# Performance work log

Measured on AMD Instinct MI355X. Metric: run time of the kernel, lower is better.

## Reference

```python
import jax, jax.numpy as jnp
import numpy as np

G, K, CG = 4, 9, 16        # DCNv3 groups, kernel points (3x3), channels/group
C = G * CG                 # internal channels = 64
OUT = 64                   # out_channels
B, H, W = 2, 256, 256


def _conv(x, w, b):  # NCHW / OIHW, SAME, stride 1
    y = jax.lax.conv_general_dilated(x, w, (1, 1), 'SAME',
                                     dimension_numbers=('NCHW', 'OIHW', 'NCHW'))
    return y + b[None, :, None, None]


def _fourdir2xy(sd):
    # rotate the two diagonal SD gradient channels by 45 deg into x/y gradients
    d0, d1 = sd[:, 0:1], sd[:, 1:2]
    return (d0 + d1) * 0.5, (d1 - d0) * 0.5


def _poisson(gx, gy, iters=20):
    # laplacian_blending_1c_batch: Jacobi Poisson solve from gradient field
    z = jnp.zeros_like(gx[:, :, :, :1])
    dgx = gx - jnp.concatenate([z, gx[:, :, :, :-1]], axis=3)
    zy = jnp.zeros_like(gy[:, :, :1, :])
    dgy = gy - jnp.concatenate([zy, gy[:, :, :-1, :]], axis=2)
    div = dgx + dgy

    def step(i, u):
        up = jnp.pad(u, ((0, 0), (0, 0), (1, 1), (1, 1)), mode='edge')
        nbr = (up[:, :, :-2, 1:-1] + up[:, :, 2:, 1:-1]
               + up[:, :, 1:-1, :-2] + up[:, :, 1:-1, 2:])
        return (nbr - div) * 0.25

    return jax.lax.fori_loop(0, iters, step, jnp.zeros_like(div))


def _dcnv3(cop, aop, W_in, b_in, W_aop, b_aop, dw, W_off, b_off,
           W_mask, b_mask, W_out, b_out):
    # channels-last DCNv3: COP provides features, AOP drives offsets/masks
    x = cop @ W_in + b_in                      # [B,H,W,C]
    a = jax.nn.gelu(aop @ W_aop + b_aop)       # [B,H,W,C]
    a = jax.lax.conv_general_dilated(a, dw, (1, 1), 'SAME',
                                     dimension_numbers=('NHWC', 'HWIO', 'NHWC'),
                                     feature_group_count=C)
    a = jax.nn.gelu(a)
    Bn, Hn, Wn = x.shape[0], x.shape[1], x.shape[2]
    off = (a @ W_off + b_off).reshape(Bn, Hn, Wn, G, K, 2)
    m = jax.nn.softmax((a @ W_mask + b_mask).reshape(Bn, Hn, Wn, G, K), axis=-1)
    xg = x.reshape(Bn, Hn, Wn, G, CG)
    yy, xx = jnp.meshgrid(jnp.arange(Hn, dtype=x.dtype),
                          jnp.arange(Wn, dtype=x.dtype), indexing='ij')
    k = jnp.arange(K)
    pky = (k // 3 - 1).astype(x.dtype)
    pkx = (k % 3 - 1).astype(x.dtype)
    ly = yy[None, :, :, None, None] + pky[None, None, None, None, :] + off[..., 0]
    lx = xx[None, :, :, None, None] + pkx[None, None, None, None, :] + off[..., 1]
    y0 = jnp.floor(ly)
    x0 = jnp.floor(lx)
    wy = ly - y0
    wx = lx - x0
    bi = jnp.arange(Bn)[:, None, None, None, None]
    gi = jnp.arange(G)[None, None, None, :, None]
    acc = jnp.zeros((Bn, Hn, Wn, G, CG), dtype=x.dtype)
    for dy, dx in ((0, 0), (0, 1), (1, 0), (1, 1)):
        yi = y0 + dy
        xi = x0 + dx
        wgt = (wy if dy else 1 - wy) * (wx if dx else 1 - wx)
        valid = ((yi >= 0) & (yi < Hn) & (xi >= 0) & (xi < Wn)).astype(x.dtype)
        yc = jnp.clip(yi, 0, Hn - 1).astype(jnp.int32)
        xc = jnp.clip(xi, 0, Wn - 1).astype(jnp.int32)
        v = xg[bi, yc, xc, gi]                  # [B,H,W,G,K,CG] gather
        acc = acc + jnp.einsum('bhwgk,bhwgkc->bhwgc', m * wgt * valid, v)
    return acc.reshape(Bn, Hn, Wn, C) @ W_out + b_out


def _forward(x, rw1, rb1, rw2, rb2, rw3, rb3, W_in, b_in, W_aop, b_aop, dw,
             W_off, b_off, W_mask, b_mask, W_out, b_out):
    img0 = x[:, 0:3]
    td = x[:, 3:5]
    sd1 = x[:, 5:7]
    sd0 = x[:, 7:9]
    Ix1, Iy1 = _fourdir2xy(sd1)
    gray = _poisson(-Ix1, -Iy1, 20)            # [B,1,H,W]
    h = jax.nn.silu(_conv(jnp.concatenate([img0, td, sd1], axis=1), rw1, rb1))
    h = jax.nn.silu(_conv(h, rw2, rb2))
    recon = _conv(h, rw3, rb3)                 # [B,3,H,W]
    core = jax.lax.stop_gradient(jnp.concatenate([img0, gray, recon], axis=1))
    guide = jax.lax.stop_gradient(jnp.concatenate([sd0, sd1], axis=1))
    cop = jnp.transpose(core, (0, 2, 3, 1))    # [B,H,W,7]
    aop = jnp.transpose(guide, (0, 2, 3, 1))   # [B,H,W,4]
    out = _dcnv3(cop, aop, W_in, b_in, W_aop, b_aop, dw, W_off, b_off,
                 W_mask, b_mask, W_out, b_out)
    return jnp.transpose(out, (0, 3, 1, 2))    # [B,OUT,H,W]


def setup_inputs() -> dict:
    key = jax.random.key(0)
    ks = jax.random.split(key, 20)
    d = {}
    d['x'] = jax.random.normal(ks[0], (B, 9, H, W), dtype=jnp.float32)
    # recon CNN (7 -> 32 -> 32 -> 3)
    d['rw1'] = jax.random.normal(ks[1], (32, 7, 3, 3), dtype=jnp.float32) * 0.1
    d['rb1'] = jnp.zeros((32,), jnp.float32)
    d['rw2'] = jax.random.normal(ks[2], (32, 32, 3, 3), dtype=jnp.float32) * 0.1
    d['rb2'] = jnp.zeros((32,), jnp.float32)
    d['rw3'] = jax.random.normal(ks[3], (3, 32, 3, 3), dtype=jnp.float32) * 0.1
    d['rb3'] = jnp.zeros((3,), jnp.float32)
    # DCNv3_Mod params
    d['W_in'] = jax.random.normal(ks[4], (7, C), dtype=jnp.float32) * 0.1
    d['b_in'] = jnp.zeros((C,), jnp.float32)
    d['W_aop'] = jax.random.normal(ks[5], (4, C), dtype=jnp.float32) * 0.1
    d['b_aop'] = jnp.zeros((C,), jnp.float32)
    d['dw'] = jax.random.normal(ks[6], (3, 3, 1, C), dtype=jnp.float32) * 0.1
    d['W_off'] = jax.random.normal(ks[7], (C, G * K * 2), dtype=jnp.float32) * 0.01
    d['b_off'] = jnp.zeros((G * K * 2,), jnp.float32)
    d['W_mask'] = jax.random.normal(ks[8], (C, G * K), dtype=jnp.float32) * 0.1
    d['b_mask'] = jnp.zeros((G * K,), jnp.float32)
    d['W_out'] = jax.random.normal(ks[9], (C, OUT), dtype=jnp.float32) * 0.1
    d['b_out'] = jnp.zeros((OUT,), jnp.float32)
    return d


def reference(x, rw1, rb1, rw2, rb2, rw3, rb3, W_in, b_in, W_aop, b_aop, dw,
              W_off, b_off, W_mask, b_mask, W_out, b_out):
    return _forward(x, rw1, rb1, rw2, rb2, rw3, rb3, W_in, b_in, W_aop, b_aop,
                    dw, W_off, b_off, W_mask, b_mask, W_out, b_out)
```

## Files before the change

### kernel.cpp

```cpp
#include <hip/hip_runtime.h>
#include <math.h>

#define H_ 256
#define W_ 256
#define HW_ 65536
#define BHW_ 131072
#define NPC 8388608

typedef __attribute__((ext_vector_type(8))) short short8v;
typedef __attribute__((ext_vector_type(4))) float f32x4;

__device__ __forceinline__ float geluf(float x) {
    const float k2 = 2.f * 0.7978845608028654f;
    float t2 = k2 * (x + 0.044715f * x * x * x);
    return x / (1.f + __expf(-t2));
}
__device__ __forceinline__ float siluf(float x) {
    return x / (1.f + __expf(-x));
}
__device__ __forceinline__ unsigned short f2bf(float f) {
    unsigned u = __float_as_uint(f);
    u = (u + 0x7FFF + ((u >> 16) & 1)) >> 16;
    return (unsigned short)u;
}

__device__ __forceinline__ float wcomb(const float* Woff, const float* Wmask, int c, int j) {
    return j < 72 ? Woff[c * 72 + j] : (j < 108 ? Wmask[c * 36 + (j - 72)] : 0.f);
}

__global__ __launch_bounds__(256) void k_mega(const float* __restrict__ x,
        float* __restrict__ gray,
        const float* __restrict__ Wa, const float* __restrict__ ba,
        const float* __restrict__ dwW, float* __restrict__ a2,
        const float* __restrict__ rw1, const float* __restrict__ rb1,
        float* __restrict__ h1,
        const float* __restrict__ Woff, const float* __restrict__ boff,
        const float* __restrict__ Wmask, const float* __restrict__ bmask,
        const float* __restrict__ Wout, const float* __restrict__ rw2,
        const float* __restrict__ rw3,
        unsigned short* __restrict__ WBpack, unsigned short* __restrict__ WOpack,
        unsigned short* __restrict__ WB2,
        float* __restrict__ bcomb, float* __restrict__ wT3) {
    __shared__ float smem[6400];
    int bid = blockIdx.x;
    int tid = threadIdx.x;

    if (bid < 512) {
        float* u = smem;
        float* dv = smem + 3192;
        int b = bid >> 8, t = bid & 255;
        int qy = t >> 4, qx = t & 15;
        int y0i = qy << 4, x0i = qx << 4;
        int ys = max(y0i - 20, 0), ye = min(y0i + 35, 255);
        int xs = max(x0i - 20, 0), xe = min(x0i + 35, 255);
        int Ht = ye - ys + 1, Wt = xe - xs + 1;
        int ty = tid >> 5, tx = tid & 31;
        const float* x5 = x + ((size_t)(b * 9 + 5) << 16);
        const float* x6 = x + ((size_t)(b * 9 + 6) << 16);

        for (int yy = ty; yy < Ht; yy += 8)
            for (int xx = tx; xx < Wt; xx += 32) {
                int gy = ys + yy, gx = xs + xx;
                int i00 = (gy << 8) + gx;
                float v5 = x5[i00], v6 = x6[i00];
                float d = -0.5f * (v5 + v6) + 0.5f * (v5 - v6);
                if (gx > 0) d += 0.5f * (x5[i00 - 1] + x6[i00 - 1]);
                if (gy > 0) d -= 0.5f * (x5[i00 - 256] - x6[i00 - 256]);
                dv[yy * 57 + xx] = d;
                u[yy * 57 + xx] = 0.f;
            }
        __syncthreads();

        float nv[7][2];
        for (int it = 0; it < 20; ++it) {
            int r = 19 - it;
            int by0 = max(y0i - r, 0), by1 = min(y0i + 15 + r, 255);
            int bx0 = max(x0i - r, 0), bx1 = min(x0i + 15 + r, 255);
            #pragma unroll
            for (int i = 0; i < 7; ++i) {
                int yy = ty + i * 8;
                int gy = ys + yy;
                #pragma unroll
                for (int j = 0; j < 2; ++j) {
                    int xx = tx + j * 32;
                    int gx = xs + xx;
                    if (gy >= by0 && gy <= by1 && gx >= bx0 && gx <= bx1) {
                        int ym = (gy > 0 ? gy - 1 : 0) - ys;
                        int yp = (gy < 255 ? gy + 1 : 255) - ys;
                        int xm = (gx > 0 ? gx - 1 : 0) - xs;
                        int xp = (gx < 255 ? gx + 1 : 255) - xs;
                        nv[i][j] = (u[ym * 57 + xx] + u[yp * 57 + xx] +
                                    u[yy * 57 + xm] + u[yy * 57 + xp] - dv[yy * 57 + xx]) * 0.25f;
                    }
                }
            }
            __syncthreads();
            #pragma unroll
            for (int i = 0; i < 7; ++i) {
                int yy = ty + i * 8;
                int gy = ys + yy;
                #pragma unroll
                for (int j = 0; j < 2; ++j) {
                    int xx = tx + j * 32;
                    int gx = xs + xx;
                    if (gy >= by0 && gy <= by1 && gx >= bx0 && gx <= bx1)
                        u[yy * 57 + xx] = nv[i][j];
                }
            }
            __syncthreads();
        }

        int oy = tid >> 4, ox = tid & 15;
        int gy = y0i + oy, gx = x0i + ox;
        gray[((size_t)b << 16) + (gy << 8) + gx] = u[(gy - ys) * 57 + (gx - xs)];

    } else if (bid < 2560) {
        float (*at)[64] = (float (*)[64])smem;
        int abid = bid - 512;
        int b = abid >> 10, tb = abid & 1023;
        int ty0 = (tb >> 5) << 3, tx0 = (tb & 31) << 3;
        const float* g0p = x + ((size_t)(b * 9 + 7) << 16);
        const float* g1p = x + ((size_t)(b * 9 + 8) << 16);
        const float* g2p = x + ((size_t)(b * 9 + 5) << 16);
        const float* g3p = x + ((size_t)(b * 9 + 6) << 16);
        int c = tid & 63;
        float w0 = Wa[c], w1 = Wa[64 + c], w2 = Wa[128 + c], w3 = Wa[192 + c];
        float bb = ba[c];
        #pragma unroll
        for (int rep = 0; rep < 25; ++rep) {
            int pos = rep * 4 + (tid >> 6);
            int py = pos / 10, pxx = pos - py * 10;
            int gy = ty0 - 1 + py, gx = tx0 - 1 + pxx;
            float v = 0.f;
            if ((unsigned)gy < 256u && (unsigned)gx < 256u) {
                int ii = (gy << 8) + gx;
                float tv = bb + g0p[ii] * w0 + g1p[ii] * w1 + g2p[ii] * w2 + g3p[ii] * w3;
                v = geluf(tv);
            }
            at[pos][c] = v;
        }
        __syncthreads();
        float dwr[9];
        #pragma unroll
        for (int k = 0; k < 9; ++k) dwr[k] = dwW[k * 64 + c];
        int pgrp = tid >> 6;
        #pragma unroll
        for (int i = 0; i < 16; ++i) {
            int pl = pgrp * 16 + i;
            int pyl = pl >> 3, pxl = pl & 7;
            float s = 0.f;
            #pragma unroll
            for (int kh = 0; kh < 3; ++kh)
                #pragma unroll
                for (int kw = 0; kw < 3; ++kw)
                    s += at[(pyl + kh) * 10 + (pxl + kw)][c] * dwr[kh * 3 + kw];
            int gy = ty0 + pyl, gx = tx0 + pxl;
            a2[(((size_t)(b << 16) + (gy << 8) + gx) << 6) + c] = geluf(s);
        }

    } else if (bid < 3072) {
        float* wsT = smem;
        for (int j = tid; j < 2016; j += 256) {
            int wb = j >> 5, o = j & 31;
            wsT[j] = rw1[o * 63 + wb];
        }
        __syncthreads();
        int cbid = bid - 2560;
        int wid = (cbid * 256 + tid) >> 6;
        int lane = tid & 63;
        int pix0 = wid << 6;
        int b = pix0 >> 16, hw0 = pix0 & 65535;
        int h = hw0 >> 8, w0 = hw0 & 255;
        float acc[32];
        #pragma unroll
        for (int o = 0; o < 32; ++o) acc[o] = rb1[o];
        const float* inb = x + ((size_t)(b * 9) << 16);
        #pragma unroll
        for (int kh = 0; kh < 3; ++kh) {
            int y = h + kh - 1;
            if ((unsigned)y >= 256u) continue;
            #pragma unroll
            for (int kw = 0; kw < 3; ++kw) {
                int xx = w0 + lane + kw - 1;
                bool valid = (unsigned)xx < 256u;
                int xc = min(max(xx, 0), 255);
                const float* p0 = inb + (y << 8) + xc;
                #pragma unroll
                for (int ci = 0; ci < 7; ++ci) {
                    float v = p0[ci << 16];
                    v = valid ? v : 0.f;
                    const float* wr = &wsT[(ci * 9 + kh * 3 + kw) * 32];
                    #pragma unroll
                    for (int o = 0; o < 32; ++o) acc[o] = fmaf(v, wr[o], acc[o]);
                }
            }
        }
        #pragma unroll
        for (int o = 0; o < 32; ++o)
            h1[((size_t)(b * 32 + o) << 16) + hw0 + lane] = siluf(acc[o]);

    } else {
        for (int idx = tid; idx < 8192; idx += 256) {
            int j = idx & 7, l = (idx >> 3) & 63, s = (idx >> 9) & 1, t = idx >> 10;
            int c = s * 32 + ((l >> 4) << 3) + j;
            int col = t * 16 + (l & 15);
            WBpack[idx] = f2bf(wcomb(Woff, Wmask, c, col));
        }
        for (int idx = tid; idx < 4096; idx += 256) {
            int j = idx & 7, l = (idx >> 3) & 63, s = (idx >> 9) & 1, t = (idx >> 10) & 3;
            int c = s * 32 + ((l >> 4) << 3) + j;
            int col = t * 16 + (l & 15);
            WOpack[idx] = f2bf(Wout[c * 64 + col]);
        }
        for (int idx = tid; idx < 9216; idx += 256) {
            int j = idx & 7, l = (idx >> 3) & 63, t = (idx >> 9) & 1, kk = idx >> 10;
            int o = t * 16 + (l & 15);
            int ci = ((l >> 4) << 3) + j;
            WB2[idx] = f2bf(rw2[o * 288 + ci * 9 + kk]);
        }
        if (tid < 128) bcomb[tid] = tid < 72 ? boff[tid] : (tid < 108 ? bmask[tid - 72] : 0.f);
        for (int j = tid; j < 288 * 3; j += 256) {
            int jj = j / 3, o = j - jj * 3;
            wT3[j] = rw3[o * 288 + jj];
        }
    }
}

__global__ __launch_bounds__(256) void k_conv2m(const float* __restrict__ h1,
        const unsigned short* __restrict__ WB2, const float* __restrict__ bias,
        float* __restrict__ h2) {
    int tid = threadIdx.x;
    int wave = tid >> 6, lane = tid & 63;
    int pix0 = (blockIdx.x << 6) + (wave << 4);
    int b = pix0 >> 16, hw0 = pix0 & 65535;
    int h = hw0 >> 8, w0 = hw0 & 255;
    int px = lane & 15, kg = lane >> 4;
    const float* inb = h1 + ((size_t)(b * 32) << 16);

    short8v af[9][2];
    #pragma unroll
    for (int kk = 0; kk < 9; ++kk) {
        af[kk][0] = *(const short8v*)&WB2[kk * 1024 + (lane << 3)];
        af[kk][1] = *(const short8v*)&WB2[kk * 1024 + 512 + (lane << 3)];
    }

    f32x4 acc0 = {0.f, 0.f, 0.f, 0.f};
    f32x4 acc1 = {0.f, 0.f, 0.f, 0.f};
    #pragma unroll
    for (int kh = 0; kh < 3; ++kh) {
        int y = h + kh - 1;
        if ((unsigned)y >= 256u) continue;
        #pragma unroll
        for (int kw = 0; kw < 3; ++kw) {
            int xx = w0 + px + kw - 1;
            bool valid = (unsigned)xx < 256u;
            int xc = min(max(xx, 0), 255);
            const float* p0 = inb + (y << 8) + xc + ((size_t)kg << 19);
            short8v bfv;
            #pragma unroll
            for (int j = 0; j < 8; ++j) {
                float v = p0[(size_t)j << 16];
                v = valid ? v : 0.f;
                bfv[j] = (short)f2bf(v);
            }
            int kk = kh * 3 + kw;
            acc0 = __builtin_amdgcn_mfma_f32_16x16x32_bf16(af[kk][0], bfv, acc0, 0, 0, 0);
            acc1 = __builtin_amdgcn_mfma_f32_16x16x32_bf16(af[kk][1], bfv, acc1, 0, 0, 0);
        }
    }
    size_t outb = ((size_t)(b * 32) << 16) + (size_t)(hw0 + px);
    #pragma unroll
    for (int r = 0; r < 4; ++r) {
        int o = (kg << 2) + r;
        h2[outb + ((size_t)o << 16)] = siluf(acc0[r] + bias[o]);
        h2[outb + ((size_t)(o + 16) << 16)] = siluf(acc1[r] + bias[o + 16]);
    }
}

__global__ __launch_bounds__(256) void k_c3x(const float* __restrict__ x,
        const float* __restrict__ gray, const float* __restrict__ h2,
        const float* __restrict__ wT3, const float* __restrict__ rb3,
        const float* __restrict__ Wi, const float* __restrict__ bi,
        float* __restrict__ xg) {
    __shared__ float st[7][256];
    int tid = threadIdx.x;
    int pixbase = blockIdx.x << 8;
    int pix = pixbase + tid;
    int b = pix >> 16, hw = pix & 65535;
    int h = hw >> 8, w = hw & 255;

    float a0 = rb3[0], a1 = rb3[1], a2v = rb3[2];
    const float* inb = h2 + ((size_t)(b * 32) << 16);
    #pragma unroll
    for (int kh = 0; kh < 3; ++kh) {
        int y = h + kh - 1;
        if ((unsigned)y >= 256u) continue;
        #pragma unroll
        for (int kw = 0; kw < 3; ++kw) {
            int xx = w + kw - 1;
            bool valid = (unsigned)xx < 256u;
            int xc = min(max(xx, 0), 255);
            const float* p0 = inb + (y << 8) + xc;
            #pragma unroll 8
            for (int ci = 0; ci < 32; ++ci) {
                float v = p0[ci << 16];
                v = valid ? v : 0.f;
                const float* wr = wT3 + (ci * 9 + kh * 3 + kw) * 3;
                a0 = fmaf(v, wr[0], a0);
                a1 = fmaf(v, wr[1], a1);
                a2v = fmaf(v, wr[2], a2v);
            }
        }
    }
    st[0][tid] = x[((size_t)(b * 9 + 0) << 16) + hw];
    st[1][tid] = x[((size_t)(b * 9 + 1) << 16) + hw];
    st[2][tid] = x[((size_t)(b * 9 + 2) << 16) + hw];
    st[3][tid] = gray[pix];
    st[4][tid] = a0;
    st[5][tid] = a1;
    st[6][tid] = a2v;
    __syncthreads();

    int c = tid & 63, sub = tid >> 6;
    float w0 = Wi[c], w1 = Wi[64 + c], w2 = Wi[128 + c], w3 = Wi[192 + c];
    float w4 = Wi[256 + c], w5 = Wi[320 + c], w6 = Wi[384 + c];
    float bb = bi[c];
    #pragma unroll 4
    for (int rep = 0; rep < 64; ++rep) {
        int pl = rep * 4 + sub;
        float v = bb + st[0][pl] * w0 + st[1][pl] * w1 + st[2][pl] * w2
                + st[3][pl] * w3 + st[4][pl] * w4 + st[5][pl] * w5 + st[6][pl] * w6;
        xg[(((size_t)(pixbase + pl)) << 6) + c] = v;
    }
}

__global__ __launch_bounds__(256, 4) void k_dcn(
        const float* __restrict__ a2, const float* __restrict__ xg,
        const unsigned short* __restrict__ WBpack,
        const unsigned short* __restrict__ WOpack,
        const float* __restrict__ bcomb, const float* __restrict__ bout,
        float* __restrict__ out) {
    __shared__ __attribute__((aligned(16))) unsigned short a2bf[16][72];
    __shared__ __attribute__((aligned(16))) unsigned short accbf[16][72];
    __shared__ __attribute__((aligned(16))) float offs[16][72];
    __shared__ float pms[16][36];
    __shared__ float invs[16][4];
    __shared__ __attribute__((aligned(16))) float taps[16][36][8];
    float (*outs)[65] = (float (*)[65])&taps[0][0][0];

    int tid = threadIdx.x;
    int wave = tid >> 6, lane = tid & 63;
    int pixbase = blockIdx.x << 4;
    int b = pixbase >> 16, hw0 = pixbase & 65535;
    int h = hw0 >> 8, w0 = hw0 & 255;
    int pw = wave << 2;

    #pragma unroll
    for (int p = 0; p < 4; ++p)
        a2bf[pw + p][lane] = f2bf(a2[((size_t)(pixbase + pw + p) << 6) + lane]);
    __syncthreads();

    {
        const unsigned short* arow = &a2bf[lane & 15][(lane >> 4) << 3];
        short8v af0 = *(const short8v*)arow;
        short8v af1 = *(const short8v*)(arow + 32);
        #pragma unroll
        for (int t2 = 0; t2 < 2; ++t2) {
            int t = 2 * wave + t2;
            int col = t * 16 + (lane & 15);
            float bc = bcomb[col];
            f32x4 acc = {bc, bc, bc, bc};
            short8v b0 = *(const short8v*)&WBpack[((t * 2 + 0) * 64 + lane) << 3];
            short8v b1 = *(const short8v*)&WBpack[((t * 2 + 1) * 64 + lane) << 3];
            acc = __builtin_amdgcn_mfma_f32_16x16x32_bf16(af0, b0, acc, 0, 0, 0);
            acc = __builtin_amdgcn_mfma_f32_16x16x32_bf16(af1, b1, acc, 0, 0, 0);
            int pxb = (lane >> 4) << 2;
            #pragma unroll
            for (int r = 0; r < 4; ++r) {
                float v = acc[r];
                int px = pxb + r;
                if (col < 72) offs[px][col] = v;
                else if (col < 108) pms[px][col - 72] = __expf(v);
            }
        }
    }
    __syncthreads();

    if (lane < 16) {
        int p = lane >> 2, g = lane & 3;
        const float* m = &pms[pw + p][g * 9];
        float s = m[0]+m[1]+m[2]+m[3]+m[4]+m[5]+m[6]+m[7]+m[8];
        invs[pw + p][g] = 1.f / s;
    }
    #pragma unroll
    for (int rep = 0; rep < 3; ++rep) {
        int idx = rep * 64 + lane;
        if (idx < 144) {
            int p = idx / 36, j = idx - p * 36;
            int px = pw + p;
            int g = j / 9, k = j - g * 9;
            float2 oxy = ((const float2*)&offs[px][0])[j];
            float pm = pms[px][j] * invs[px][g];
            float ly = (float)(h + k / 3 - 1) + oxy.x;
            float lx = (float)(w0 + px + (k % 3) - 1) + oxy.y;
            float y0f = floorf(ly), x0f = floorf(lx);
            float wy = ly - y0f, wx = lx - x0f;
            int iy0 = (int)y0f, ix0 = (int)x0f;
            int base = b << 16;
            float4 t01, t23;
            {
                int yi = iy0, xi = ix0;
                float wgt = (1.f - wy) * (1.f - wx) * pm;
                if (yi < 0 || yi > 255 || xi < 0 || xi > 255) wgt = 0.f;
                int yc = min(max(yi, 0), 255), xc = min(max(xi, 0), 255);
                t01.x = __int_as_float((base + (yc << 8) + xc) << 8); t01.y = wgt;
            }
            {
                int yi = iy0, xi = ix0 + 1;
                float wgt = (1.f - wy) * wx * pm;
                if (yi < 0 || yi > 255 || xi < 0 || xi > 255) wgt = 0.f;
                int yc = min(max(yi, 0), 255), xc = min(max(xi, 0), 255);
                t01.z = __int_as_float((base + (yc << 8) + xc) << 8); t01.w = wgt;
            }
            {
                int yi = iy0 + 1, xi = ix0;
                float wgt = wy * (1.f - wx) * pm;
                if (yi < 0 || yi > 255 || xi < 0 || xi > 255) wgt = 0.f;
                int yc = min(max(yi, 0), 255), xc = min(max(xi, 0), 255);
                t23.x = __int_as_float((base + (yc << 8) + xc) << 8); t23.y = wgt;
            }
            {
                int yi = iy0 + 1, xi = ix0 + 1;
                float wgt = wy * wx * pm;
                if (yi < 0 || yi > 255 || xi < 0 || xi > 255) wgt = 0.f;
                int yc = min(max(yi, 0), 255), xc = min(max(xi, 0), 255);
                t23.z = __int_as_float((base + (yc << 8) + xc) << 8); t23.w = wgt;
            }
            ((float4*)&taps[px][j][0])[0] = t01;
            ((float4*)&taps[px][j][0])[1] = t23;
        }
    }
    {
        int g4 = lane >> 4;
        const char* xgb = (const char*)xg;
        unsigned lane4 = (unsigned)(lane << 2);
        #pragma unroll
        for (int p = 0; p < 4; ++p) {
            float acc = 0.f;
            const float4* tp = (const float4*)&taps[pw + p][g4 * 9][0];
            #pragma unroll
            for (int k = 0; k < 9; ++k) {
                float4 d0 = tp[2 * k], d1 = tp[2 * k + 1];
                acc = fmaf(d0.y, *(const float*)(xgb + ((unsigned)__float_as_int(d0.x) + lane4)), acc);
                acc = fmaf(d0.w, *(const float*)(xgb + ((unsigned)__float_as_int(d0.z) + lane4)), acc);
                acc = fmaf(d1.y, *(const float*)(xgb + ((unsigned)__float_as_int(d1.x) + lane4)), acc);
                acc = fmaf(d1.w, *(const float*)(xgb + ((unsigned)__float_as_int(d1.z) + lane4)), acc);
            }
            accbf[pw + p][lane] = f2bf(acc);
        }
    }
    __syncthreads();

    {
        const unsigned short* arow = &accbf[lane & 15][(lane >> 4) << 3];
        short8v hf0 = *(const short8v*)arow;
        short8v hf1 = *(const short8v*)(arow + 32);
        int t = wave;
        int col = t * 16 + (lane & 15);
        float bo = bout[col];
        f32x4 acc = {bo, bo, bo, bo};
        short8v w0v = *(const short8v*)&WOpack[((t * 2 + 0) * 64 + lane) << 3];
        short8v w1v = *(const short8v*)&WOpack[((t * 2 + 1) * 64 + lane) << 3];
        acc = __builtin_amdgcn_mfma_f32_16x16x32_bf16(hf0, w0v, acc, 0, 0, 0);
        acc = __builtin_amdgcn_mfma_f32_16x16x32_bf16(hf1, w1v, acc, 0, 0, 0);
        int pxb = (lane >> 4) << 2;
        #pragma unroll
        for (int r = 0; r < 4; ++r)
            outs[pxb + r][col] = acc[r];
    }
    __syncthreads();

    int cq = tid >> 4, px = tid & 15;
    size_t rowb = ((size_t)(b * 64) << 16) + hw0 + px;
    #pragma unroll
    for (int rep = 0; rep < 4; ++rep) {
        int c = cq + rep * 16;
        out[rowb + ((size_t)c << 16)] = outs[px][c];
    }
}

extern "C" void kernel_launch(void* const* d_in, const int* in_sizes, int n_in,
                              void* d_out, int out_size, void* d_ws, size_t ws_size,
                              hipStream_t stream) {
    const float* x      = (const float*)d_in[0];
    const float* rw1    = (const float*)d_in[1];
    const float* rb1    = (const float*)d_in[2];
    const float* rw2    = (const float*)d_in[3];
    const float* rb2    = (const float*)d_in[4];
    const float* rw3    = (const float*)d_in[5];
    const float* rb3    = (const float*)d_in[6];
    const float* W_in   = (const float*)d_in[7];
    const float* b_in   = (const float*)d_in[8];
    const float* W_aop  = (const float*)d_in[9];
    const float* b_aop  = (const float*)d_in[10];
    const float* dw     = (const float*)d_in[11];
    const float* W_off  = (const float*)d_in[12];
    const float* b_off  = (const float*)d_in[13];
    const float* W_mask = (const float*)d_in[14];
    const float* b_mask = (const float*)d_in[15];
    const float* W_out  = (const float*)d_in[16];
    const float* b_out  = (const float*)d_in[17];
    float* out = (float*)d_out;

    float* ws = (float*)d_ws;
    float* gray  = ws;
    float* h1    = gray + BHW_;
    float* h2    = h1 + (size_t)BHW_ * 32;
    float* a2    = h2 + (size_t)BHW_ * 32;
    float* xg    = a2 + (size_t)NPC;
    float* bcomb = xg + (size_t)NPC;
    float* wT3   = bcomb + 128;
    unsigned short* WBpack = (unsigned short*)(wT3 + 864);
    unsigned short* WOpack = WBpack + 8192;
    unsigned short* WB2    = WOpack + 4096;

    dim3 blk(256);

    k_mega<<<dim3(3073), blk, 0, stream>>>(x, gray, W_aop, b_aop, dw, a2,
                                           rw1, rb1, h1,
                                           W_off, b_off, W_mask, b_mask, W_out,
                                           rw2, rw3,
                                           WBpack, WOpack, WB2, bcomb, wT3);
    k_conv2m<<<dim3(BHW_ / 64), blk, 0, stream>>>(h1, WB2, rb2, h2);
    k_c3x<<<dim3(BHW_ / 256), blk, 0, stream>>>(x, gray, h2, wT3, rb3,
                                                W_in, b_in, xg);
    k_dcn<<<dim3(BHW_ / 16), blk, 0, stream>>>(a2, xg, WBpack, WOpack,
                                               bcomb, b_out, out);
}
```

Measured before the change: 162.9 us.

## Shrink mega-kernel LDS, keep divergence in registers, vectorize deformable gather

The Poisson tile keeps its divergence values in per-thread registers instead of shared memory. The depthwise staging tile is stored as bf16, which halves the mega-kernel's shared memory from 6400 to 3200 floats and should allow more resident blocks per CU. In the deformable sampling kernel, each lane now gathers two adjacent channels with a float2 load and handles two pixels per pass, which halves the number of gather instructions. In exchange, the depthwise inputs are rounded to bf16 and the Poisson threads need more registers.

```diff
diff --git a/kernel.cpp b/kernel.cpp
--- a/kernel.cpp
+++ b/kernel.cpp
@@ -22,6 +22,9 @@
     unsigned u = __float_as_uint(f);
     u = (u + 0x7FFF + ((u >> 16) & 1)) >> 16;
     return (unsigned short)u;
+}
+__device__ __forceinline__ float bf2f(unsigned short s) {
+    return __uint_as_float((unsigned)s << 16);
 }
 
 __device__ __forceinline__ float wcomb(const float* Woff, const float* Wmask, int c, int j) {
@@ -41,13 +44,12 @@
         unsigned short* __restrict__ WBpack, unsigned short* __restrict__ WOpack,
         unsigned short* __restrict__ WB2,
         float* __restrict__ bcomb, float* __restrict__ wT3) {
-    __shared__ float smem[6400];
+    __shared__ float smem[3200];
     int bid = blockIdx.x;
     int tid = threadIdx.x;
 
     if (bid < 512) {
         float* u = smem;
-        float* dv = smem + 3192;
         int b = bid >> 8, t = bid & 255;
         int qy = t >> 4, qx = t & 15;
         int y0i = qy << 4, x0i = qx << 4;
@@ -58,17 +60,25 @@
         const float* x5 = x + ((size_t)(b * 9 + 5) << 16);
         const float* x6 = x + ((size_t)(b * 9 + 6) << 16);
 
-        for (int yy = ty; yy < Ht; yy += 8)
-            for (int xx = tx; xx < Wt; xx += 32) {
-                int gy = ys + yy, gx = xs + xx;
-                int i00 = (gy << 8) + gx;
-                float v5 = x5[i00], v6 = x6[i00];
-                float d = -0.5f * (v5 + v6) + 0.5f * (v5 - v6);
-                if (gx > 0) d += 0.5f * (x5[i00 - 1] + x6[i00 - 1]);
-                if (gy > 0) d -= 0.5f * (x5[i00 - 256] - x6[i00 - 256]);
-                dv[yy * 57 + xx] = d;
-                u[yy * 57 + xx] = 0.f;
-            }
+        float dvr[7][2];
+        #pragma unroll
+        for (int i = 0; i < 7; ++i) {
+            int yy = ty + i * 8;
+            #pragma unroll
+            for (int j = 0; j < 2; ++j) {
+                int xx = tx + j * 32;
+                if (yy < Ht && xx < Wt) {
+                    int gy = ys + yy, gx = xs + xx;
+                    int i00 = (gy << 8) + gx;
+                    float v5 = x5[i00], v6 = x6[i00];
+                    float d = -0.5f * (v5 + v6) + 0.5f * (v5 - v6);
+                    if (gx > 0) d += 0.5f * (x5[i00 - 1] + x6[i00 - 1]);
+                    if (gy > 0) d -= 0.5f * (x5[i00 - 256] - x6[i00 - 256]);
+                    dvr[i][j] = d;
+                    u[yy * 57 + xx] = 0.f;
+                }
+            }
+        }
         __syncthreads();
 
         float nv[7][2];
@@ -90,7 +100,7 @@
                         int xm = (gx > 0 ? gx - 1 : 0) - xs;
                         int xp = (gx < 255 ? gx + 1 : 255) - xs;
                         nv[i][j] = (u[ym * 57 + xx] + u[yp * 57 + xx] +
-                                    u[yy * 57 + xm] + u[yy * 57 + xp] - dv[yy * 57 + xx]) * 0.25f;
+                                    u[yy * 57 + xm] + u[yy * 57 + xp] - dvr[i][j]) * 0.25f;
                     }
                 }
             }
@@ -115,7 +125,7 @@
         gray[((size_t)b << 16) + (gy << 8) + gx] = u[(gy - ys) * 57 + (gx - xs)];
 
     } else if (bid < 2560) {
-        float (*at)[64] = (float (*)[64])smem;
+        unsigned short (*at)[64] = (unsigned short (*)[64])smem;
         int abid = bid - 512;
         int b = abid >> 10, tb = abid & 1023;
         int ty0 = (tb >> 5) << 3, tx0 = (tb & 31) << 3;
@@ -137,7 +147,7 @@
                 float tv = bb + g0p[ii] * w0 + g1p[ii] * w1 + g2p[ii] * w2 + g3p[ii] * w3;
                 v = geluf(tv);
             }
-            at[pos][c] = v;
+            at[pos][c] = f2bf(v);
         }
         __syncthreads();
         float dwr[9];
@@ -153,7 +163,7 @@
             for (int kh = 0; kh < 3; ++kh)
                 #pragma unroll
                 for (int kw = 0; kw < 3; ++kw)
-                    s += at[(pyl + kh) * 10 + (pxl + kw)][c] * dwr[kh * 3 + kw];
+                    s += bf2f(at[(pyl + kh) * 10 + (pxl + kw)][c]) * dwr[kh * 3 + kw];
             int gy = ty0 + pyl, gx = tx0 + pxl;
             a2[(((size_t)(b << 16) + (gy << 8) + gx) << 6) + c] = geluf(s);
         }
@@ -441,22 +451,37 @@
         }
     }
     {
-        int g4 = lane >> 4;
+        int cp = lane & 31, px2 = lane >> 5;
+        int g9 = (cp >> 3) * 9;
         const char* xgb = (const char*)xg;
-        unsigned lane4 = (unsigned)(lane << 2);
-        #pragma unroll
-        for (int p = 0; p < 4; ++p) {
-            float acc = 0.f;
-            const float4* tp = (const float4*)&taps[pw + p][g4 * 9][0];
+        unsigned cp8 = (unsigned)(cp << 3);
+        #pragma unroll
+        for (int pr = 0; pr < 2; ++pr) {
+            int px = pw + pr * 2 + px2;
+            float ax = 0.f, ay = 0.f;
+            const float4* tp4 = (const float4*)&taps[px][g9][0];
             #pragma unroll
             for (int k = 0; k < 9; ++k) {
-                float4 d0 = tp[2 * k], d1 = tp[2 * k + 1];
-                acc = fmaf(d0.y, *(const float*)(xgb + ((unsigned)__float_as_int(d0.x) + lane4)), acc);
-                acc = fmaf(d0.w, *(const float*)(xgb + ((unsigned)__float_as_int(d0.z) + lane4)), acc);
-                acc = fmaf(d1.y, *(const float*)(xgb + ((unsigned)__float_as_int(d1.x) + lane4)), acc);
-                acc = fmaf(d1.w, *(const float*)(xgb + ((unsigned)__float_as_int(d1.z) + lane4)), acc);
-            }
-            accbf[pw + p][lane] = f2bf(acc);
+                float4 d0 = tp4[2 * k], d1 = tp4[2 * k + 1];
+                {
+                    float2 v = *(const float2*)(xgb + ((unsigned)__float_as_int(d0.x) + cp8));
+                    ax = fmaf(d0.y, v.x, ax); ay = fmaf(d0.y, v.y, ay);
+                }
+                {
+                    float2 v = *(const float2*)(xgb + ((unsigned)__float_as_int(d0.z) + cp8));
+                    ax = fmaf(d0.w, v.x, ax); ay = fmaf(d0.w, v.y, ay);
+                }
+                {
+                    float2 v = *(const float2*)(xgb + ((unsigned)__float_as_int(d1.x) + cp8));
+                    ax = fmaf(d1.y, v.x, ax); ay = fmaf(d1.y, v.y, ay);
+                }
+                {
+                    float2 v = *(const float2*)(xgb + ((unsigned)__float_as_int(d1.z) + cp8));
+                    ax = fmaf(d1.w, v.x, ax); ay = fmaf(d1.w, v.y, ay);
+                }
+            }
+            unsigned packed = (unsigned)f2bf(ax) | ((unsigned)f2bf(ay) << 16);
+            *(unsigned*)&accbf[px][cp << 1] = packed;
         }
     }
     __syncthreads();
```

After: 190.9 us. 1.17x slower.
